# Optimization experiments

Measured on AMD Instinct MI355X. Metric: run time of the kernel, lower is better.

The kernel has to match this reference:

```python
import jax, jax.numpy as jnp
import numpy as np

B, S, T = 256, 2048, 48  # batch, seq_len, num_tags


def setup_inputs() -> dict:
    key = jax.random.key(0)
    k1, k2, k3 = jax.random.split(key, 3)
    emissions = jax.random.normal(k1, (B, S, T), dtype=jnp.float32)
    tags = jax.random.randint(k2, (B, S), 0, T)
    mask = jnp.ones((B, S), dtype=bool)
    transitions = jax.random.uniform(k3, (T, T), minval=-0.1, maxval=0.1, dtype=jnp.float32)
    return {"emissions": emissions, "tags": tags, "mask": mask, "transitions": transitions}


def _crf_llh(emissions, transitions, tags, mask):
    # --- numerator: score of the gold path (fully vectorized over time) ---
    maskf = mask.astype(emissions.dtype)
    emit = jnp.take_along_axis(emissions, tags[:, :, None], axis=2)[..., 0]  # (B,S)
    trans = transitions[tags[:, :-1], tags[:, 1:]]                            # (B,S-1)
    numerator = emit[:, 0] + ((trans + emit[:, 1:]) * maskf[:, 1:]).sum(axis=1)  # (B,)

    # --- denominator: forward algorithm (logsumexp recurrence) via lax.scan ---
    def step(score, x):
        e_i, m_i = x  # (B,T), (B,)
        # score[b,j] -> logsumexp_j( score[b,j] + transitions[j,k] ) + e_i[b,k]
        nxt = jax.nn.logsumexp(score[:, :, None] + transitions[None, :, :]
                               + e_i[:, None, :], axis=1)  # (B,T)
        score = jnp.where(m_i[:, None], nxt, score)
        return score, None

    init = emissions[:, 0]  # (B,T)
    xs = (jnp.swapaxes(emissions[:, 1:], 0, 1),  # (S-1,B,T)
          jnp.swapaxes(mask[:, 1:], 0, 1))       # (S-1,B)
    final, _ = jax.lax.scan(step, init, xs)
    denominator = jax.nn.logsumexp(final, axis=1)  # (B,)

    llh = numerator - denominator  # (B,)
    return llh.mean()  # reduction='mean' (torch default)


def reference(emissions, tags, mask, transitions):
    return _crf_llh(emissions, transitions, tags, mask)
```

## Files before the change

kernel.cpp:

```cpp
#include <hip/hip_runtime.h>

#define TT 48
#define SS 2048
#define BB 256
#define NP 128
#define SL 16
#define WU 8
#define NWAVE ((BB * NP) / 16)
#define LN2 0.69314718056f

typedef float f32x4 __attribute__((ext_vector_type(4)));
typedef short bf16x8 __attribute__((ext_vector_type(8)));
typedef int i32x4 __attribute__((ext_vector_type(4)));

__device__ __forceinline__ float wave_sum64(float v) {
#pragma unroll
  for (int off = 32; off > 0; off >>= 1) v += __shfl_xor(v, off, 64);
  return v;
}
__device__ __forceinline__ unsigned short bf16rne(float x) {
  unsigned b = __float_as_uint(x);
  b += 0x7fffu + ((b >> 16) & 1u);
  return (unsigned short)(b >> 16);
}
__device__ __forceinline__ bf16x8 pack8(f32x4 lo, f32x4 hi) {
  bf16x8 r;
  r[0] = (short)bf16rne(lo.x); r[1] = (short)bf16rne(lo.y);
  r[2] = (short)bf16rne(lo.z); r[3] = (short)bf16rne(lo.w);
  r[4] = (short)bf16rne(hi.x); r[5] = (short)bf16rne(hi.y);
  r[6] = (short)bf16rne(hi.z); r[7] = (short)bf16rne(hi.w);
  return r;
}
__device__ __forceinline__ f32x4 mfma(bf16x8 a, bf16x8 b, f32x4 c) {
  return __builtin_amdgcn_mfma_f32_16x16x32_bf16(a, b, c, 0, 0, 0);
}
__device__ __forceinline__ unsigned pktr(float lo, float hi) {
  return __builtin_amdgcn_perm(__float_as_uint(hi), __float_as_uint(lo),
                               0x07060302u);
}
#define EXPW(A)                           \
  { A.x = __expf(A.x); A.y = __expf(A.y); \
    A.z = __expf(A.z); A.w = __expf(A.w); }

#define LOADBANK(BK, S0)                                     \
  {                                                          \
    _Pragma("unroll")                                        \
    for (int k_ = 0; k_ < 4; ++k_) {                         \
      int s_ = (S0) + k_;                                    \
      s_ = s_ < SS ? s_ : SS - 1;                            \
      const float* pe_ = eb + (size_t)s_ * TT;               \
      BK[k_][0] = *(const float4*)(pe_ + 0);                 \
      BK[k_][1] = *(const float4*)(pe_ + 16);                \
      BK[k_][2] = *(const float4*)(pe_ + 32);                \
    }                                                        \
  }

#define CSTEP(TV, ST, DOREN, MEAS)                                          \
  {                                                                         \
    f32x4 d0 = mfma(Af[0][1], Bc1, mfma(Af[0][0], Bc0, zz));                \
    f32x4 d1 = mfma(Af[1][1], Bc1, mfma(Af[1][0], Bc0, zz));                \
    f32x4 d2 = mfma(Af[2][1], Bc1, mfma(Af[2][0], Bc0, zz));                \
    float4 t0 = TV[ST][0], t1 = TV[ST][1], t2 = TV[ST][2];                  \
    EXPW(t0); EXPW(t1); EXPW(t2);                                           \
    f32x4 tt0 = {t0.x, t0.y, t0.z, t0.w};                                   \
    f32x4 tt1 = {t1.x, t1.y, t1.z, t1.w};                                   \
    f32x4 tt2 = {t2.x, t2.y, t2.z, t2.w};                                   \
    if (DOREN) {                                                            \
      K += kp;                                                              \
      float sc_ = __int_as_float((127 - kp) << 23);                         \
      tt0 *= sc_; tt1 *= sc_; tt2 *= sc_;                                   \
    }                                                                       \
    W0 = d0 * tt0; W1 = d1 * tt1; W2 = d2 * tt2;                            \
    i32x4 p0_ = {(int)pktr(W0.x, W0.y), (int)pktr(W0.z, W0.w),              \
                 (int)pktr(W1.x, W1.y), (int)pktr(W1.z, W1.w)};             \
    Bc0 = __builtin_bit_cast(bf16x8, p0_);                                  \
    i32x4 p1_ = {(int)pktr(W2.x, W2.y), (int)pktr(W2.z, W2.w), 0, 0};       \
    Bc1 = __builtin_bit_cast(bf16x8, p1_);                                  \
    if (MEAS) {                                                             \
      float lm = fmaxf(fmaxf(fmaxf(W0.x, W0.y), fmaxf(W0.z, W0.w)),         \
                       fmaxf(fmaxf(fmaxf(W1.x, W1.y), fmaxf(W1.z, W1.w)),   \
                             fmaxf(fmaxf(W2.x, W2.y), fmaxf(W2.z, W2.w)))); \
      lm = fmaxf(lm, __shfl_xor(lm, 16, 64));                               \
      lm = fmaxf(lm, __shfl_xor(lm, 32, 64));                               \
      int kr = ((__float_as_int(lm) >> 23) & 0xff) - 127;                   \
      kp = kr < -126 ? -126 : (kr > 126 ? 126 : kr);                        \
    }                                                                       \
  }

#define COLSUM_LOG(LOUT)                                                 \
  {                                                                      \
    float s_ = ((W0.x + W0.y) + (W0.z + W0.w)) +                         \
               ((W1.x + W1.y) + (W1.z + W1.w)) +                         \
               ((W2.x + W2.y) + (W2.z + W2.w));                          \
    s_ += __shfl_xor(s_, 16, 64);                                        \
    s_ += __shfl_xor(s_, 32, 64);                                        \
    LOUT = __logf(s_) + (float)K * LN2;                                  \
  }

__global__ __launch_bounds__(64, 2) void seg_kernel(
    const float* __restrict__ emis, const int* __restrict__ tags,
    const float* __restrict__ trans, float* __restrict__ rho,
    float* __restrict__ num) {
  const int lane = threadIdx.x;

  if (blockIdx.x >= NWAVE) {
    const int b = blockIdx.x - NWAVE;
    const float* ebb = emis + (size_t)b * SS * TT;
    const int* tb = tags + b * SS;
    float acc = 0.f;
    for (int s = lane; s < SS; s += 64) {
      int tg = tb[s];
      acc += ebb[(size_t)s * TT + tg];
      if (s > 0) acc += trans[tb[s - 1] * TT + tg];
    }
    acc = wave_sum64(acc);
    if (lane == 0) num[b] = acc;
    return;
  }

  const int col = lane & 15;
  const int g = lane >> 4;
  const int G = blockIdx.x * 16 + col;
  const int p = G >> 8;
  const int b = G & 255;
  const int sbase = 1 + p * SL;
  const int wstart = (p == 0) ? 1 : sbase - WU;
  const f32x4 zz = {0.f, 0.f, 0.f, 0.f};

  bf16x8 Af[3][2];
#pragma unroll
  for (int ti = 0; ti < 3; ++ti) {
    const int j = 16 * ti + col;
    f32x4 lo, hi;
    lo.x = __expf(trans[(4 * g + 0) * TT + j]);
    lo.y = __expf(trans[(4 * g + 1) * TT + j]);
    lo.z = __expf(trans[(4 * g + 2) * TT + j]);
    lo.w = __expf(trans[(4 * g + 3) * TT + j]);
    hi.x = __expf(trans[(16 + 4 * g + 0) * TT + j]);
    hi.y = __expf(trans[(16 + 4 * g + 1) * TT + j]);
    hi.z = __expf(trans[(16 + 4 * g + 2) * TT + j]);
    hi.w = __expf(trans[(16 + 4 * g + 3) * TT + j]);
    Af[ti][0] = pack8(lo, hi);
    lo.x = __expf(trans[(32 + 4 * g + 0) * TT + j]);
    lo.y = __expf(trans[(32 + 4 * g + 1) * TT + j]);
    lo.z = __expf(trans[(32 + 4 * g + 2) * TT + j]);
    lo.w = __expf(trans[(32 + 4 * g + 3) * TT + j]);
    Af[ti][1] = pack8(lo, zz);
  }

  const float* eb = emis + (size_t)b * SS * TT + 4 * g;

  bf16x8 Bc0, Bc1;
  if (p == 0) {
    float4 a0 = *(const float4*)(eb + 0);
    float4 a1 = *(const float4*)(eb + 16);
    float4 a2 = *(const float4*)(eb + 32);
    EXPW(a0); EXPW(a1); EXPW(a2);
    f32x4 b0 = {a0.x, a0.y, a0.z, a0.w};
    f32x4 b1 = {a1.x, a1.y, a1.z, a1.w};
    f32x4 b2 = {a2.x, a2.y, a2.z, a2.w};
    Bc0 = pack8(b0, b1);
    Bc1 = pack8(b2, zz);
  } else {
#pragma unroll
    for (int e = 0; e < 8; ++e) {
      Bc0[e] = (short)0x3F80;
      Bc1[e] = (short)((e < 4) ? 0x3F80 : 0);
    }
  }

  f32x4 W0 = zz, W1 = zz, W2 = zz;
  int K = 0, kp = 0;
  float Lb = 0.f, Le;
  float4 tA[4][3], tB[4][3];

  LOADBANK(tA, wstart);
  LOADBANK(tB, wstart + 4);
  CSTEP(tA, 0, 0, 0);
  CSTEP(tA, 1, 0, 0);
  CSTEP(tA, 2, 0, 0);
  CSTEP(tA, 3, 0, 0);
  LOADBANK(tA, wstart + 8);
  CSTEP(tB, 0, 0, 0);
  CSTEP(tB, 1, 0, 0);
  CSTEP(tB, 2, 0, 0);
  CSTEP(tB, 3, 0, 1);
  if (p > 0) { COLSUM_LOG(Lb); }
  LOADBANK(tB, wstart + 12);
  CSTEP(tA, 0, 1, 0);
  CSTEP(tA, 1, 0, 0);
  CSTEP(tA, 2, 0, 0);
  CSTEP(tA, 3, 0, 0);
  LOADBANK(tA, wstart + 16);
  CSTEP(tB, 0, 0, 0);
  CSTEP(tB, 1, 0, 0);
  CSTEP(tB, 2, 0, 0);
  CSTEP(tB, 3, 0, 1);
  if (p > 0) {
    LOADBANK(tB, wstart + 20);
    CSTEP(tA, 0, 1, 0);
    CSTEP(tA, 1, 0, 0);
    CSTEP(tA, 2, 0, 0);
    CSTEP(tA, 3, 0, 0);
    CSTEP(tB, 0, 0, 0);
    CSTEP(tB, 1, 0, 0);
    CSTEP(tB, 2, 0, 0);
    if (p < NP - 1) { CSTEP(tB, 3, 0, 0); }
  }
  COLSUM_LOG(Le);

  if (g == 0) rho[G] = (p == 0) ? Le : (Le - Lb);
}

__global__ void final_kernel(const float* __restrict__ rho,
                             const float* __restrict__ num,
                             float* __restrict__ out) {
  const int t = threadIdx.x;
  float den = 0.f;
#pragma unroll 8
  for (int p = 0; p < NP; ++p) den += rho[p * BB + t];
  float v = num[t] - den;
  v = wave_sum64(v);
  __shared__ float red[4];
  if ((t & 63) == 0) red[t >> 6] = v;
  __syncthreads();
  if (t == 0) out[0] = ((red[0] + red[1]) + (red[2] + red[3])) * (1.f / BB);
}

extern "C" void kernel_launch(void* const* d_in, const int* in_sizes, int n_in,
                              void* d_out, int out_size, void* d_ws, size_t ws_size,
                              hipStream_t stream) {
  const float* emis = (const float*)d_in[0];
  const int* tags = (const int*)d_in[1];
  const float* trans = (const float*)d_in[3];
  float* rho = (float*)d_ws;
  float* num = rho + NP * BB;
  seg_kernel<<<NWAVE + BB, 64, 0, stream>>>(emis, tags, trans, rho, num);
  final_kernel<<<1, 256, 0, stream>>>(rho, num, (float*)d_out);
}
```

Measured before the change: 55.87 us.

## Stage emission tiles through LDS with coalesced per-batch row loads

Instead of each lane gathering scattered float4s from its own batch row, 48 lanes now load contiguous 4-step windows (192 floats) for each of 16 batch elements. These go into a padded shared-memory buffer, and each column then reads its own slices back out. The goal is better global-load coalescing and fewer scattered transactions. The cost is LDS round trips, and there is no explicit barrier, which relies on the block being a single 64-lane wave. The block-to-(p,b) mapping also changes so that the 16 columns share the same p.

New measurement: 95.23 us. +70.5%, slower.

```diff
diff --git a/kernel.cpp b/kernel.cpp
--- a/kernel.cpp
+++ b/kernel.cpp
@@ -8,6 +8,7 @@
 #define WU 8
 #define NWAVE ((BB * NP) / 16)
 #define LN2 0.69314718056f
+#define LSTRIDE 51
 
 typedef float f32x4 __attribute__((ext_vector_type(4)));
 typedef short bf16x8 __attribute__((ext_vector_type(8)));
@@ -41,19 +42,6 @@
 #define EXPW(A)                           \
   { A.x = __expf(A.x); A.y = __expf(A.y); \
     A.z = __expf(A.z); A.w = __expf(A.w); }
-
-#define LOADBANK(BK, S0)                                     \
-  {                                                          \
-    _Pragma("unroll")                                        \
-    for (int k_ = 0; k_ < 4; ++k_) {                         \
-      int s_ = (S0) + k_;                                    \
-      s_ = s_ < SS ? s_ : SS - 1;                            \
-      const float* pe_ = eb + (size_t)s_ * TT;               \
-      BK[k_][0] = *(const float4*)(pe_ + 0);                 \
-      BK[k_][1] = *(const float4*)(pe_ + 16);                \
-      BK[k_][2] = *(const float4*)(pe_ + 32);                \
-    }                                                        \
-  }
 
 #define CSTEP(TV, ST, DOREN, MEAS)                                          \
   {                                                                         \
@@ -97,6 +85,39 @@
     LOUT = __logf(s_) + (float)K * LN2;                                  \
   }
 
+#define PLOADW(R, W)                                                  \
+  if (lane < 48) {                                                    \
+    const int s0_ = wstart + 4 * (W);                                 \
+    int sr_ = s0_ + rl;                                               \
+    sr_ = sr_ < SS ? sr_ : SS - 1;                                    \
+    const size_t off_ = (size_t)sr_ * TT + fl;                        \
+    _Pragma("unroll")                                                 \
+    for (int ci = 0; ci < 16; ++ci)                                   \
+      R[ci] = *(const float4*)(ebase + (size_t)ci * SS * TT + off_);  \
+  }
+
+#define DSW(R)                                   \
+  if (lane < 48) {                               \
+    _Pragma("unroll")                            \
+    for (int ci = 0; ci < 16; ++ci)              \
+      sbuf[ci * LSTRIDE + lane] = R[ci];         \
+  }
+
+#define CONSW(NST, D0, M3)                                          \
+  {                                                                 \
+    float4 tv[4][3];                                                \
+    _Pragma("unroll")                                               \
+    for (int r_ = 0; r_ < (NST); ++r_) {                            \
+      tv[r_][0] = sbuf[col * LSTRIDE + r_ * 12 + 0 + g];            \
+      tv[r_][1] = sbuf[col * LSTRIDE + r_ * 12 + 4 + g];            \
+      tv[r_][2] = sbuf[col * LSTRIDE + r_ * 12 + 8 + g];            \
+    }                                                               \
+    CSTEP(tv, 0, D0, 0);                                            \
+    if ((NST) > 1) CSTEP(tv, 1, 0, 0);                              \
+    if ((NST) > 2) CSTEP(tv, 2, 0, 0);                              \
+    if ((NST) > 3) CSTEP(tv, 3, 0, M3);                             \
+  }
+
 __global__ __launch_bounds__(64, 2) void seg_kernel(
     const float* __restrict__ emis, const int* __restrict__ tags,
     const float* __restrict__ trans, float* __restrict__ rho,
@@ -118,13 +139,18 @@
     return;
   }
 
+  __shared__ __align__(16) float4 sbuf[16 * LSTRIDE];
+
   const int col = lane & 15;
   const int g = lane >> 4;
   const int G = blockIdx.x * 16 + col;
-  const int p = G >> 8;
-  const int b = G & 255;
-  const int sbase = 1 + p * SL;
-  const int wstart = (p == 0) ? 1 : sbase - WU;
+  const int p = blockIdx.x >> 4;
+  const int b0 = (blockIdx.x & 15) * 16;
+  const int b = b0 + col;
+  const int wstart = (p == 0) ? 1 : (1 + p * SL - WU);
+  const int rl = lane / 12;
+  const int fl = (lane % 12) * 4;
+  const float* ebase = emis + (size_t)b0 * SS * TT;
   const f32x4 zz = {0.f, 0.f, 0.f, 0.f};
 
   bf16x8 Af[3][2];
@@ -148,19 +174,18 @@
     Af[ti][1] = pack8(lo, zz);
   }
 
-  const float* eb = emis + (size_t)b * SS * TT + 4 * g;
-
   bf16x8 Bc0, Bc1;
   if (p == 0) {
-    float4 a0 = *(const float4*)(eb + 0);
-    float4 a1 = *(const float4*)(eb + 16);
-    float4 a2 = *(const float4*)(eb + 32);
+    const float* e0 = emis + (size_t)b * SS * TT + 4 * g;
+    float4 a0 = *(const float4*)(e0 + 0);
+    float4 a1 = *(const float4*)(e0 + 16);
+    float4 a2 = *(const float4*)(e0 + 32);
     EXPW(a0); EXPW(a1); EXPW(a2);
-    f32x4 b0 = {a0.x, a0.y, a0.z, a0.w};
-    f32x4 b1 = {a1.x, a1.y, a1.z, a1.w};
-    f32x4 b2 = {a2.x, a2.y, a2.z, a2.w};
-    Bc0 = pack8(b0, b1);
-    Bc1 = pack8(b2, zz);
+    f32x4 v0 = {a0.x, a0.y, a0.z, a0.w};
+    f32x4 v1 = {a1.x, a1.y, a1.z, a1.w};
+    f32x4 v2 = {a2.x, a2.y, a2.z, a2.w};
+    Bc0 = pack8(v0, v1);
+    Bc1 = pack8(v2, zz);
   } else {
 #pragma unroll
     for (int e = 0; e < 8; ++e) {
@@ -172,40 +197,27 @@
   f32x4 W0 = zz, W1 = zz, W2 = zz;
   int K = 0, kp = 0;
   float Lb = 0.f, Le;
-  float4 tA[4][3], tB[4][3];
-
-  LOADBANK(tA, wstart);
-  LOADBANK(tB, wstart + 4);
-  CSTEP(tA, 0, 0, 0);
-  CSTEP(tA, 1, 0, 0);
-  CSTEP(tA, 2, 0, 0);
-  CSTEP(tA, 3, 0, 0);
-  LOADBANK(tA, wstart + 8);
-  CSTEP(tB, 0, 0, 0);
-  CSTEP(tB, 1, 0, 0);
-  CSTEP(tB, 2, 0, 0);
-  CSTEP(tB, 3, 0, 1);
+  float4 RA[16], RB[16];
+
+  PLOADW(RA, 0);
+  PLOADW(RB, 1);
+  DSW(RA); CONSW(4, 0, 0);
+  PLOADW(RA, 2);
+  DSW(RB); CONSW(4, 0, 1);
   if (p > 0) { COLSUM_LOG(Lb); }
-  LOADBANK(tB, wstart + 12);
-  CSTEP(tA, 0, 1, 0);
-  CSTEP(tA, 1, 0, 0);
-  CSTEP(tA, 2, 0, 0);
-  CSTEP(tA, 3, 0, 0);
-  LOADBANK(tA, wstart + 16);
-  CSTEP(tB, 0, 0, 0);
-  CSTEP(tB, 1, 0, 0);
-  CSTEP(tB, 2, 0, 0);
-  CSTEP(tB, 3, 0, 1);
+  PLOADW(RB, 3);
+  DSW(RA); CONSW(4, 1, 0);
+  if (p > 0) { PLOADW(RA, 4); }
+  DSW(RB); CONSW(4, 0, 1);
   if (p > 0) {
-    LOADBANK(tB, wstart + 20);
-    CSTEP(tA, 0, 1, 0);
-    CSTEP(tA, 1, 0, 0);
-    CSTEP(tA, 2, 0, 0);
-    CSTEP(tA, 3, 0, 0);
-    CSTEP(tB, 0, 0, 0);
-    CSTEP(tB, 1, 0, 0);
-    CSTEP(tB, 2, 0, 0);
-    if (p < NP - 1) { CSTEP(tB, 3, 0, 0); }
+    PLOADW(RB, 5);
+    DSW(RA); CONSW(4, 1, 0);
+    DSW(RB);
+    if (p < NP - 1) {
+      CONSW(4, 0, 0);
+    } else {
+      CONSW(3, 0, 0);
+    }
   }
   COLSUM_LOG(Le);
 
```

## Halve segment length to double parallel segments, remap waves per batch

Applied to the files above, without the earlier changes.

Splits the sequence into 256 segments of 8 steps instead of 128 of 16, so each wave runs a shorter serial MFMA chain with the same 8-step warmup. Each wave now covers 16 consecutive segments of a single batch row rather than 16 batch rows of one segment. The first segment is handled by 16 extra dedicated waves. This targets per-wave latency at the cost of twice as many waves and proportionally more redundant warmup work and emission reads.

After: 72.70 us. +30.1%, slower.

```diff
diff --git a/kernel.cpp b/kernel.cpp
--- a/kernel.cpp
+++ b/kernel.cpp
@@ -3,10 +3,11 @@
 #define TT 48
 #define SS 2048
 #define BB 256
-#define NP 128
-#define SL 16
+#define NP 256
+#define SL 8
 #define WU 8
 #define NWAVE ((BB * NP) / 16)
+#define NEX 16
 #define LN2 0.69314718056f
 
 typedef float f32x4 __attribute__((ext_vector_type(4)));
@@ -42,29 +43,15 @@
   { A.x = __expf(A.x); A.y = __expf(A.y); \
     A.z = __expf(A.z); A.w = __expf(A.w); }
 
-#define LOADBANK(BK, S0)                                     \
-  {                                                          \
-    _Pragma("unroll")                                        \
-    for (int k_ = 0; k_ < 4; ++k_) {                         \
-      int s_ = (S0) + k_;                                    \
-      s_ = s_ < SS ? s_ : SS - 1;                            \
-      const float* pe_ = eb + (size_t)s_ * TT;               \
-      BK[k_][0] = *(const float4*)(pe_ + 0);                 \
-      BK[k_][1] = *(const float4*)(pe_ + 16);                \
-      BK[k_][2] = *(const float4*)(pe_ + 32);                \
-    }                                                        \
-  }
-
-#define CSTEP(TV, ST, DOREN, MEAS)                                          \
+#define CSTEP(T0, T1, T2, DOREN, MEAS)                                      \
   {                                                                         \
     f32x4 d0 = mfma(Af[0][1], Bc1, mfma(Af[0][0], Bc0, zz));                \
     f32x4 d1 = mfma(Af[1][1], Bc1, mfma(Af[1][0], Bc0, zz));                \
     f32x4 d2 = mfma(Af[2][1], Bc1, mfma(Af[2][0], Bc0, zz));                \
-    float4 t0 = TV[ST][0], t1 = TV[ST][1], t2 = TV[ST][2];                  \
-    EXPW(t0); EXPW(t1); EXPW(t2);                                           \
-    f32x4 tt0 = {t0.x, t0.y, t0.z, t0.w};                                   \
-    f32x4 tt1 = {t1.x, t1.y, t1.z, t1.w};                                   \
-    f32x4 tt2 = {t2.x, t2.y, t2.z, t2.w};                                   \
+    EXPW(T0); EXPW(T1); EXPW(T2);                                           \
+    f32x4 tt0 = {T0.x, T0.y, T0.z, T0.w};                                   \
+    f32x4 tt1 = {T1.x, T1.y, T1.z, T1.w};                                   \
+    f32x4 tt2 = {T2.x, T2.y, T2.z, T2.w};                                   \
     if (DOREN) {                                                            \
       K += kp;                                                              \
       float sc_ = __int_as_float((127 - kp) << 23);                         \
@@ -97,14 +84,33 @@
     LOUT = __logf(s_) + (float)K * LN2;                                  \
   }
 
+#define LOADBANK(BK, L0)                                     \
+  {                                                          \
+    _Pragma("unroll")                                        \
+    for (int k_ = 0; k_ < 4; ++k_) {                         \
+      int s_ = ws + (L0) + k_;                               \
+      s_ = s_ < 0 ? 0 : (s_ < SS ? s_ : SS - 1);             \
+      const float* pe_ = eb + (size_t)s_ * TT;               \
+      BK[k_][0] = *(const float4*)(pe_ + 0);                 \
+      BK[k_][1] = *(const float4*)(pe_ + 16);                \
+      BK[k_][2] = *(const float4*)(pe_ + 32);                \
+    }                                                        \
+  }
+
+#define WIN4(BK, D0, ML)                                          \
+  { _Pragma("unroll")                                             \
+    for (int r_ = 0; r_ < 4; ++r_)                                \
+      CSTEP(BK[r_][0], BK[r_][1], BK[r_][2],                      \
+            (r_ == 0) && (D0), (r_ == 3) && (ML)) }
+
 __global__ __launch_bounds__(64, 2) void seg_kernel(
     const float* __restrict__ emis, const int* __restrict__ tags,
     const float* __restrict__ trans, float* __restrict__ rho,
     float* __restrict__ num) {
   const int lane = threadIdx.x;
 
-  if (blockIdx.x >= NWAVE) {
-    const int b = blockIdx.x - NWAVE;
+  if (blockIdx.x >= NWAVE + NEX) {
+    const int b = blockIdx.x - NWAVE - NEX;
     const float* ebb = emis + (size_t)b * SS * TT;
     const int* tb = tags + b * SS;
     float acc = 0.f;
@@ -120,11 +126,6 @@
 
   const int col = lane & 15;
   const int g = lane >> 4;
-  const int G = blockIdx.x * 16 + col;
-  const int p = G >> 8;
-  const int b = G & 255;
-  const int sbase = 1 + p * SL;
-  const int wstart = (p == 0) ? 1 : sbase - WU;
   const f32x4 zz = {0.f, 0.f, 0.f, 0.f};
 
   bf16x8 Af[3][2];
@@ -148,68 +149,67 @@
     Af[ti][1] = pack8(lo, zz);
   }
 
-  const float* eb = emis + (size_t)b * SS * TT + 4 * g;
-
   bf16x8 Bc0, Bc1;
-  if (p == 0) {
-    float4 a0 = *(const float4*)(eb + 0);
-    float4 a1 = *(const float4*)(eb + 16);
-    float4 a2 = *(const float4*)(eb + 32);
-    EXPW(a0); EXPW(a1); EXPW(a2);
-    f32x4 b0 = {a0.x, a0.y, a0.z, a0.w};
-    f32x4 b1 = {a1.x, a1.y, a1.z, a1.w};
-    f32x4 b2 = {a2.x, a2.y, a2.z, a2.w};
-    Bc0 = pack8(b0, b1);
-    Bc1 = pack8(b2, zz);
-  } else {
+  f32x4 W0 = zz, W1 = zz, W2 = zz;
+  int K = 0, kp = 0;
+
+  if (blockIdx.x < NWAVE) {
+    const int b = blockIdx.x >> 4;
+    const int q = blockIdx.x & 15;
+    const int pc = q * 16 + col;
+    const int ws = pc * SL - (WU - 1);
+    const float* eb = emis + (size_t)b * SS * TT + 4 * g;
+
 #pragma unroll
     for (int e = 0; e < 8; ++e) {
       Bc0[e] = (short)0x3F80;
       Bc1[e] = (short)((e < 4) ? 0x3F80 : 0);
     }
-  }
-
-  f32x4 W0 = zz, W1 = zz, W2 = zz;
-  int K = 0, kp = 0;
-  float Lb = 0.f, Le;
-  float4 tA[4][3], tB[4][3];
-
-  LOADBANK(tA, wstart);
-  LOADBANK(tB, wstart + 4);
-  CSTEP(tA, 0, 0, 0);
-  CSTEP(tA, 1, 0, 0);
-  CSTEP(tA, 2, 0, 0);
-  CSTEP(tA, 3, 0, 0);
-  LOADBANK(tA, wstart + 8);
-  CSTEP(tB, 0, 0, 0);
-  CSTEP(tB, 1, 0, 0);
-  CSTEP(tB, 2, 0, 0);
-  CSTEP(tB, 3, 0, 1);
-  if (p > 0) { COLSUM_LOG(Lb); }
-  LOADBANK(tB, wstart + 12);
-  CSTEP(tA, 0, 1, 0);
-  CSTEP(tA, 1, 0, 0);
-  CSTEP(tA, 2, 0, 0);
-  CSTEP(tA, 3, 0, 0);
-  LOADBANK(tA, wstart + 16);
-  CSTEP(tB, 0, 0, 0);
-  CSTEP(tB, 1, 0, 0);
-  CSTEP(tB, 2, 0, 0);
-  CSTEP(tB, 3, 0, 1);
-  if (p > 0) {
-    LOADBANK(tB, wstart + 20);
-    CSTEP(tA, 0, 1, 0);
-    CSTEP(tA, 1, 0, 0);
-    CSTEP(tA, 2, 0, 0);
-    CSTEP(tA, 3, 0, 0);
-    CSTEP(tB, 0, 0, 0);
-    CSTEP(tB, 1, 0, 0);
-    CSTEP(tB, 2, 0, 0);
-    if (p < NP - 1) { CSTEP(tB, 3, 0, 0); }
-  }
-  COLSUM_LOG(Le);
-
-  if (g == 0) rho[G] = (p == 0) ? Le : (Le - Lb);
+
+    float Lb, Le14, Le15;
+    float4 tA[4][3], tB[4][3];
+    LOADBANK(tA, 0);
+    LOADBANK(tB, 4);
+    WIN4(tA, 0, 0);
+    LOADBANK(tA, 8);
+    WIN4(tB, 0, 1);
+    COLSUM_LOG(Lb);
+    LOADBANK(tB, 12);
+    WIN4(tA, 1, 0);
+    CSTEP(tB[0][0], tB[0][1], tB[0][2], 0, 0);
+    CSTEP(tB[1][0], tB[1][1], tB[1][2], 0, 0);
+    CSTEP(tB[2][0], tB[2][1], tB[2][2], 0, 0);
+    COLSUM_LOG(Le14);
+    CSTEP(tB[3][0], tB[3][1], tB[3][2], 0, 0);
+    COLSUM_LOG(Le15);
+    float rv = ((pc == NP - 1) ? Le14 : Le15) - Lb;
+    if (g == 0 && pc > 0) rho[pc * BB + b] = rv;
+  } else {
+    const int b0 = (blockIdx.x - NWAVE) * 16;
+    const int b = b0 + col;
+    const int ws = 1;
+    const float* eb = emis + (size_t)b * SS * TT + 4 * g;
+    {
+      const float* e0 = emis + (size_t)b * SS * TT + 4 * g;
+      float4 a0 = *(const float4*)(e0 + 0);
+      float4 a1 = *(const float4*)(e0 + 16);
+      float4 a2 = *(const float4*)(e0 + 32);
+      EXPW(a0); EXPW(a1); EXPW(a2);
+      f32x4 v0 = {a0.x, a0.y, a0.z, a0.w};
+      f32x4 v1 = {a1.x, a1.y, a1.z, a1.w};
+      f32x4 v2 = {a2.x, a2.y, a2.z, a2.w};
+      Bc0 = pack8(v0, v1);
+      Bc1 = pack8(v2, zz);
+    }
+    float4 tA[4][3], tB[4][3];
+    LOADBANK(tA, 0);
+    LOADBANK(tB, 4);
+    WIN4(tA, 0, 0);
+    WIN4(tB, 0, 0);
+    float Le;
+    COLSUM_LOG(Le);
+    if (g == 0) rho[0 * BB + b] = Le;
+  }
 }
 
 __global__ void final_kernel(const float* __restrict__ rho,
@@ -235,6 +235,6 @@
   const float* trans = (const float*)d_in[3];
   float* rho = (float*)d_ws;
   float* num = rho + NP * BB;
-  seg_kernel<<<NWAVE + BB, 64, 0, stream>>>(emis, tags, trans, rho, num);
+  seg_kernel<<<NWAVE + NEX + BB, 64, 0, stream>>>(emis, tags, trans, rho, num);
   final_kernel<<<1, 256, 0, stream>>>(rho, num, (float*)d_out);
 }
```
